# Kernel optimization log

Measured on AMD Instinct MI355X. Metric: run time of the kernel, lower is better.

Reference implementation:

```python
import jax, jax.numpy as jnp
import numpy as np

NHEADS = 8
START_ID = 1
MAX_LEN = 24

def _ln(x, g, b, eps=1e-5):
    m = x.mean(-1, keepdims=True)
    v = ((x - m) ** 2).mean(-1, keepdims=True)
    return (x - m) * jax.lax.rsqrt(v + eps) * g + b

def _mha(q_in, kv_in, w, b, ow, ob, mask):
    # q_in: [Lq,B,E], kv_in: [Lk,B,E]; w: [E,3E] packed q/k/v (transposed torch in_proj)
    E = q_in.shape[-1]; H = NHEADS; D = E // H
    Lq, B = q_in.shape[0], q_in.shape[1]; Lk = kv_in.shape[0]
    q = (q_in @ w[:, :E] + b[:E]).reshape(Lq, B, H, D)
    k = (kv_in @ w[:, E:2 * E] + b[E:2 * E]).reshape(Lk, B, H, D)
    v = (kv_in @ w[:, 2 * E:] + b[2 * E:]).reshape(Lk, B, H, D)
    s = jnp.einsum('qbhd,kbhd->bhqk', q, k) * (1.0 / float(np.sqrt(D)))
    if mask is not None:
        s = s + mask
    a = jax.nn.softmax(s, axis=-1)
    o = jnp.einsum('bhqk,kbhd->qbhd', a, v).reshape(Lq, B, E)
    return o @ ow + ob

def _sinusoidal_pe(S, E):
    pos = np.arange(S)[:, None]
    div = np.exp(np.arange(0, E, 2) * (-np.log(10000.0) / E))
    pe = np.zeros((S, E), dtype=np.float32)
    pe[:, 0::2] = np.sin(pos * div)
    pe[:, 1::2] = np.cos(pos * div)
    return jnp.asarray(pe)[:, None, :]  # [S,1,E]

def _model(input_tensor, emb, enc_attn_w, enc_attn_b, enc_attn_ow, enc_attn_ob,
           enc_ln1_g, enc_ln1_b, enc_ln2_g, enc_ln2_b,
           enc_ffn_w1, enc_ffn_b1, enc_ffn_w2, enc_ffn_b2,
           enc_norm_g, enc_norm_b,
           dec_sa_w, dec_sa_b, dec_sa_ow, dec_sa_ob,
           dec_ca_w, dec_ca_b, dec_ca_ow, dec_ca_ob,
           dec_ln1_g, dec_ln1_b, dec_ln2_g, dec_ln2_b, dec_ln3_g, dec_ln3_b,
           dec_ffn_w1, dec_ffn_b1, dec_ffn_w2, dec_ffn_b2,
           dec_norm_g, dec_norm_b, voc_w, voc_b):
    E = emb.shape[1]
    B, S = input_tensor.shape
    # encoder: seq-first [S,B,E], sinusoidal PE added (decoder side gets NO PE, as in source)
    x = jnp.take(emb, input_tensor.T, axis=0) + _sinusoidal_pe(S, E)
    for l in range(enc_attn_w.shape[0]):  # post-LN encoder layers
        a = _mha(x, x, enc_attn_w[l], enc_attn_b[l], enc_attn_ow[l], enc_attn_ob[l], None)
        x = _ln(x + a, enc_ln1_g[l], enc_ln1_b[l])
        f = jax.nn.relu(x @ enc_ffn_w1[l] + enc_ffn_b1[l]) @ enc_ffn_w2[l] + enc_ffn_b2[l]
        x = _ln(x + f, enc_ln2_g[l], enc_ln2_b[l])
    memory = _ln(x, enc_norm_g, enc_norm_b)

    Lbuf = MAX_LEN + 1
    causal = jnp.where(jnp.triu(jnp.ones((Lbuf, Lbuf), jnp.float32), k=1) == 1, -jnp.inf, 0.0)

    def dec_forward(tokens):
        # full (wasteful, KV-cache-free) decoder pass over the whole token buffer,
        # matching the source's recompute-everything greedy loop; causal masking
        # makes position i identical to the source's length-(i+1) prefix pass.
        y = jnp.take(emb, tokens, axis=0)  # [Lbuf,B,E]; shared embedding, no PE (as in source)
        for l in range(dec_sa_w.shape[0]):
            a = _mha(y, y, dec_sa_w[l], dec_sa_b[l], dec_sa_ow[l], dec_sa_ob[l], causal)
            y = _ln(y + a, dec_ln1_g[l], dec_ln1_b[l])
            c = _mha(y, memory, dec_ca_w[l], dec_ca_b[l], dec_ca_ow[l], dec_ca_ob[l], None)
            y = _ln(y + c, dec_ln2_g[l], dec_ln2_b[l])
            f = jax.nn.relu(y @ dec_ffn_w1[l] + dec_ffn_b1[l]) @ dec_ffn_w2[l] + dec_ffn_b2[l]
            y = _ln(y + f, dec_ln3_g[l], dec_ln3_b[l])
        return _ln(y, dec_norm_g, dec_norm_b)

    def step(tokens, i):
        out_i = jnp.take(dec_forward(tokens), i, axis=0)  # [B,E] == out[-1] of prefix pass
        prob = out_i @ voc_w + voc_b                      # [B,V_tgt]
        nxt = jnp.argmax(prob, axis=-1).astype(tokens.dtype)
        return tokens.at[i + 1].set(nxt), (nxt, prob)

    tokens0 = jnp.full((Lbuf, B), START_ID, dtype=input_tensor.dtype)
    _, (pred_tokens, dists) = jax.lax.scan(step, tokens0, jnp.arange(MAX_LEN))
    return pred_tokens, dists  # [MAX_LEN,B] int, [MAX_LEN,B,V_tgt]


def setup_inputs() -> dict:
    V, VT, E, F, LE, LD, B, S = 32000, 32000, 512, 2048, 3, 3, 8, 24
    keys = iter(jax.random.split(jax.random.key(0), 48))
    def W(*shape):
        return jax.random.normal(next(keys), shape, jnp.float32) * 0.02
    return dict(
        input_tensor=jax.random.randint(next(keys), (B, S), 0, V),
        emb=W(V, E),
        enc_attn_w=W(LE, E, 3 * E), enc_attn_b=jnp.zeros((LE, 3 * E)),
        enc_attn_ow=W(LE, E, E), enc_attn_ob=jnp.zeros((LE, E)),
        enc_ln1_g=jnp.ones((LE, E)), enc_ln1_b=jnp.zeros((LE, E)),
        enc_ln2_g=jnp.ones((LE, E)), enc_ln2_b=jnp.zeros((LE, E)),
        enc_ffn_w1=W(LE, E, F), enc_ffn_b1=jnp.zeros((LE, F)),
        enc_ffn_w2=W(LE, F, E), enc_ffn_b2=jnp.zeros((LE, E)),
        enc_norm_g=jnp.ones((E,)), enc_norm_b=jnp.zeros((E,)),
        dec_sa_w=W(LD, E, 3 * E), dec_sa_b=jnp.zeros((LD, 3 * E)),
        dec_sa_ow=W(LD, E, E), dec_sa_ob=jnp.zeros((LD, E)),
        dec_ca_w=W(LD, E, 3 * E), dec_ca_b=jnp.zeros((LD, 3 * E)),
        dec_ca_ow=W(LD, E, E), dec_ca_ob=jnp.zeros((LD, E)),
        dec_ln1_g=jnp.ones((LD, E)), dec_ln1_b=jnp.zeros((LD, E)),
        dec_ln2_g=jnp.ones((LD, E)), dec_ln2_b=jnp.zeros((LD, E)),
        dec_ln3_g=jnp.ones((LD, E)), dec_ln3_b=jnp.zeros((LD, E)),
        dec_ffn_w1=W(LD, E, F), dec_ffn_b1=jnp.zeros((LD, F)),
        dec_ffn_w2=W(LD, F, E), dec_ffn_b2=jnp.zeros((LD, E)),
        dec_norm_g=jnp.ones((E,)), dec_norm_b=jnp.zeros((E,)),
        voc_w=W(E, VT), voc_b=jnp.zeros((VT,)),
    )


def reference(input_tensor, emb, enc_attn_w, enc_attn_b, enc_attn_ow, enc_attn_ob,
              enc_ln1_g, enc_ln1_b, enc_ln2_g, enc_ln2_b,
              enc_ffn_w1, enc_ffn_b1, enc_ffn_w2, enc_ffn_b2,
              enc_norm_g, enc_norm_b,
              dec_sa_w, dec_sa_b, dec_sa_ow, dec_sa_ob,
              dec_ca_w, dec_ca_b, dec_ca_ow, dec_ca_ob,
              dec_ln1_g, dec_ln1_b, dec_ln2_g, dec_ln2_b, dec_ln3_g, dec_ln3_b,
              dec_ffn_w1, dec_ffn_b1, dec_ffn_w2, dec_ffn_b2,
              dec_norm_g, dec_norm_b, voc_w, voc_b):
    return _model(input_tensor, emb, enc_attn_w, enc_attn_b, enc_attn_ow, enc_attn_ob,
                  enc_ln1_g, enc_ln1_b, enc_ln2_g, enc_ln2_b,
                  enc_ffn_w1, enc_ffn_b1, enc_ffn_w2, enc_ffn_b2,
                  enc_norm_g, enc_norm_b,
                  dec_sa_w, dec_sa_b, dec_sa_ow, dec_sa_ob,
                  dec_ca_w, dec_ca_b, dec_ca_ow, dec_ca_ob,
                  dec_ln1_g, dec_ln1_b, dec_ln2_g, dec_ln2_b, dec_ln3_g, dec_ln3_b,
                  dec_ffn_w1, dec_ffn_b1, dec_ffn_w2, dec_ffn_b2,
                  dec_norm_g, dec_norm_b, voc_w, voc_b)
```

## Files before the change

kernel.cpp:

```cpp
#include <hip/hip_runtime.h>
#include <stdint.h>

#define E    512
#define H    8
#define DH   64
#define BB   8
#define SS   24
#define FF   2048
#define NL   3
#define VTOK 32000
#define LBUF 25
#define ML   24
#define START_ID 1

__global__ void enc_embed_kernel(const int* __restrict__ inp, const float* __restrict__ emb,
                                 float* __restrict__ x) {
  int r = blockIdx.x;
  int s = r / BB, b = r % BB;
  int tok = inp[b * SS + s];
  const float* er = emb + (size_t)tok * E;
  for (int e = threadIdx.x; e < E; e += blockDim.x) {
    int j = e >> 1;
    double dv = exp(-((double)(2 * j)) * (log(10000.0) / (double)E));
    double ang = (double)s * dv;
    double pe = (e & 1) ? cos(ang) : sin(ang);
    x[(size_t)r * E + e] = er[e] + (float)pe;
  }
}

__global__ __launch_bounds__(256) void ln_kernel(const float* __restrict__ x,
                          const float* __restrict__ g,
                          const float* __restrict__ bta, float* __restrict__ y) {
  int r = blockIdx.x;
  int t = threadIdx.x;
  const float* xr = x + (size_t)r * E;
  float a0 = xr[t], a1 = xr[t + 256];
  __shared__ float red[256];
  red[t] = a0 + a1;
  __syncthreads();
  for (int s = 128; s > 0; s >>= 1) { if (t < s) red[t] += red[t + s]; __syncthreads(); }
  float m = red[0] * (1.0f / (float)E);
  __syncthreads();
  float d0 = a0 - m, d1 = a1 - m;
  red[t] = d0 * d0 + d1 * d1;
  __syncthreads();
  for (int s = 128; s > 0; s >>= 1) { if (t < s) red[t] += red[t + s]; __syncthreads(); }
  float v = red[0] * (1.0f / (float)E);
  float rstd = 1.0f / sqrtf(v + 1e-5f);
  y[(size_t)r * E + t]       = d0 * rstd * g[t]       + bta[t];
  y[(size_t)r * E + t + 256] = d1 * rstd * g[t + 256] + bta[t + 256];
}

__global__ __launch_bounds__(256) void fgemm_kernel(
    const float* __restrict__ A, int K,
    const float* __restrict__ W, int ldw, int N,
    const float* __restrict__ bias,
    const float* __restrict__ resid,
    float* __restrict__ C, int relu,
    unsigned long long* __restrict__ amax) {
  __shared__ float Al[8 * 512];
  __shared__ float red[16 * 512];
  int t = threadIdx.x;
  int c0 = blockIdx.x * 64;
  int s = blockIdx.y;
  int row0 = blockIdx.z * 8;
  int kbase = s * 512;
  for (int i = t; i < 1024; i += 256) {
    int r = i >> 7, cc = i & 127;
    ((float4*)Al)[i] = *(const float4*)(A + (size_t)(row0 + r) * K + kbase + (cc << 2));
  }
  __syncthreads();
  int tc = t & 15, tk = t >> 4;
  int col = c0 + (tc << 2);
  float acc[8][4];
#pragma unroll
  for (int m = 0; m < 8; ++m) { acc[m][0] = acc[m][1] = acc[m][2] = acc[m][3] = 0.f; }
  const float4* wp = (const float4*)(W + (size_t)kbase * ldw + col);
  const size_t ld4 = (size_t)(ldw >> 2);
#pragma unroll 8
  for (int i = 0; i < 32; ++i) {
    int k = tk + (i << 4);
    float4 wv = wp[(size_t)k * ld4];
#pragma unroll
    for (int m = 0; m < 8; ++m) {
      float a = Al[m * 512 + k];
      acc[m][0] += a * wv.x; acc[m][1] += a * wv.y;
      acc[m][2] += a * wv.z; acc[m][3] += a * wv.w;
    }
  }
#pragma unroll
  for (int m = 0; m < 8; ++m) {
    float4* rr = (float4*)&red[tk * 512 + m * 64 + (tc << 2)];
    *rr = make_float4(acc[m][0], acc[m][1], acc[m][2], acc[m][3]);
  }
  __syncthreads();
  float out2[2];
#pragma unroll
  for (int j = 0; j < 2; ++j) {
    int o = t + j * 256;
    float v = 0.f;
#pragma unroll
    for (int sl = 0; sl < 16; ++sl) v += red[sl * 512 + o];
    out2[j] = v;
  }
  int S = gridDim.y;
  if (S > 1) {
    int M = gridDim.z * 8;
#pragma unroll
    for (int j = 0; j < 2; ++j) {
      int o = t + j * 256; int m = o >> 6, cc = o & 63;
      C[((size_t)s * M + row0 + m) * N + c0 + cc] = out2[j];
    }
  } else {
#pragma unroll
    for (int j = 0; j < 2; ++j) {
      int o = t + j * 256; int m = o >> 6, cc = o & 63;
      int col2 = c0 + cc;
      float v = out2[j] + bias[col2];
      if (resid) v += resid[(size_t)(row0 + m) * N + col2];
      if (relu) v = fmaxf(v, 0.0f);
      C[(size_t)(row0 + m) * N + col2] = v;
      out2[j] = v;
    }
    if (amax) {
      __syncthreads();
      unsigned long long* keys = (unsigned long long*)red;
// ... 70 lines not shown
  int t = threadIdx.x;
  for (int idx = t; idx < SS * DH; idx += 256) {
    int srow = idx / DH, d = idx - srow * DH;
    size_t base = ((size_t)(srow * BB + b)) * (3 * E) + h * DH + d;
    qs[idx] = qkv[base];
    ks[idx] = qkv[base + E];
    vs[idx] = qkv[base + 2 * E];
  }
  __syncthreads();
  for (int p = t; p < SS * SS; p += 256) {
    int qi = p / SS, kj = p - qi * SS;
    float a = 0.f;
    for (int d = 0; d < DH; ++d) a += qs[qi * DH + d] * ks[kj * DH + d];
    sc[qi][kj] = a * 0.125f;
  }
  __syncthreads();
  if (t < SS) {
    float mx = -1e30f;
    for (int j = 0; j < SS; ++j) mx = fmaxf(mx, sc[t][j]);
    float sm = 0.f;
    for (int j = 0; j < SS; ++j) { float ev = expf(sc[t][j] - mx); sc[t][j] = ev; sm += ev; }
    float inv = 1.0f / sm;
    for (int j = 0; j < SS; ++j) sc[t][j] *= inv;
  }
  __syncthreads();
  for (int p = t; p < SS * DH; p += 256) {
    int qi = p / DH, d = p - qi * DH;
    float a = 0.f;
    for (int j = 0; j < SS; ++j) a += sc[qi][j] * vs[j * DH + d];
    o[((size_t)(qi * BB + b)) * E + h * DH + d] = a;
  }
}

__global__ __launch_bounds__(64) void dec_sa_attn_kernel(const float* __restrict__ qkv,
                                   float* __restrict__ Kc, float* __restrict__ Vc,
                                   float* __restrict__ o, int pos) {
  int b = blockIdx.x >> 3, h = blockIdx.x & 7;
  int t = threadIdx.x;
  const float* qp = qkv + (size_t)b * (3 * E) + h * DH;
  const float* kn = qp + E;
  const float* vn = qp + 2 * E;
  float* kc = Kc + ((size_t)pos * BB + b) * E + h * DH;
  float* vc = Vc + ((size_t)pos * BB + b) * E + h * DH;
  __shared__ float qs[DH];
  __shared__ float sc[32];
  kc[t] = kn[t]; vc[t] = vn[t]; qs[t] = qp[t];
  __syncthreads();
  int L = pos + 1;
  if (t < L) {
    const float* kr = (t == pos) ? kn : (Kc + ((size_t)t * BB + b) * E + h * DH);
    float a = 0.f;
#pragma unroll 8
    for (int d = 0; d < DH; ++d) a += qs[d] * kr[d];
    sc[t] = a * 0.125f;
  }
  __syncthreads();
  if (t == 0) {
    float mx = -1e30f;
    for (int j = 0; j < L; ++j) mx = fmaxf(mx, sc[j]);
    float sm = 0.f;
    for (int j = 0; j < L; ++j) { float ev = expf(sc[j] - mx); sc[j] = ev; sm += ev; }
    float inv = 1.0f / sm;
    for (int j = 0; j < L; ++j) sc[j] *= inv;
  }
  __syncthreads();
  float a = 0.f;
  for (int j = 0; j < L; ++j) {
    const float* vr = (j == pos) ? vn : (Vc + ((size_t)j * BB + b) * E + h * DH);
    a += sc[j] * vr[t];
  }
  o[(size_t)b * E + h * DH + t] = a;
}

__global__ __launch_bounds__(64) void dec_ca_attn_kernel(const float* __restrict__ q,
                                   const float* __restrict__ Km, const float* __restrict__ Vm,
                                   float* __restrict__ o) {
  int b = blockIdx.x >> 3, h = blockIdx.x & 7;
  int t = threadIdx.x;
  __shared__ float qs[DH];
  __shared__ float sc[SS];
  qs[t] = q[(size_t)b * E + h * DH + t];
  __syncthreads();
  if (t < SS) {
    const float* kr = Km + ((size_t)t * BB + b) * E + h * DH;
    float a = 0.f;
#pragma unroll 8
    for (int d = 0; d < DH; ++d) a += qs[d] * kr[d];
    sc[t] = a * 0.125f;
  }
  __syncthreads();
  if (t == 0) {
    float mx = -1e30f;
    for (int j = 0; j < SS; ++j) mx = fmaxf(mx, sc[j]);
    float sm = 0.f;
    for (int j = 0; j < SS; ++j) { float ev = expf(sc[j] - mx); sc[j] = ev; sm += ev; }
    float inv = 1.0f / sm;
    for (int j = 0; j < SS; ++j) sc[j] *= inv;
  }
  __syncthreads();
  float a = 0.f;
  for (int j = 0; j < SS; ++j) a += sc[j] * Vm[((size_t)j * BB + b) * E + h * DH + t];
  o[(size_t)b * E + h * DH + t] = a;
}

__global__ void dec_embed_kernel(const int* __restrict__ tokens, const float* __restrict__ emb,
                                 float* __restrict__ y, int i) {
  int b = blockIdx.x;
  int tok = tokens[i * BB + b];
  const float* er = emb + (size_t)tok * E;
  for (int e = threadIdx.x; e < E; e += blockDim.x) y[(size_t)b * E + e] = er[e];
}

__global__ void dec_init_kernel(int* __restrict__ tokens, unsigned long long* __restrict__ amax) {
  int t = threadIdx.x;
  if (t < BB) { tokens[t] = START_ID; amax[t] = 0ull; }
}

__global__ void next_token_kernel(unsigned long long* __restrict__ amax, int* __restrict__ tokens,
                                  float* __restrict__ outtok, int i) {
  int t = threadIdx.x;
  if (t < BB) {
    unsigned long long p = amax[t];
    int idx = (int)(0xFFFFFFFFu - (unsigned int)(p & 0xFFFFFFFFull));
    tokens[(i + 1) * BB + t] = idx;
    outtok[i * BB + t] = (float)idx;
    amax[t] = 0ull;
  }
}

extern "C" void kernel_launch(void* const* d_in, const int* in_sizes, int n_in,
                              void* d_out, int out_size, void* d_ws, size_t ws_size,
                              hipStream_t stream) {
  (void)in_sizes; (void)n_in; (void)out_size; (void)ws_size;
  const int*   inp   = (const int*)d_in[0];
  const float* emb   = (const float*)d_in[1];
  const float* e_aw  = (const float*)d_in[2];
  const float* e_ab  = (const float*)d_in[3];
  const float* e_aow = (const float*)d_in[4];
  const float* e_aob = (const float*)d_in[5];
  const float* e_l1g = (const float*)d_in[6];
  const float* e_l1b = (const float*)d_in[7];
  const float* e_l2g = (const float*)d_in[8];
  const float* e_l2b = (const float*)d_in[9];
// ... 3 lines not shown
  const float* e_f2b = (const float*)d_in[13];
  const float* e_ng  = (const float*)d_in[14];
  const float* e_nb  = (const float*)d_in[15];
  const float* d_saw = (const float*)d_in[16];
  const float* d_sab = (const float*)d_in[17];
  const float* d_saow= (const float*)d_in[18];
  const float* d_saob= (const float*)d_in[19];
  const float* d_caw = (const float*)d_in[20];
  const float* d_cab = (const float*)d_in[21];
  const float* d_caow= (const float*)d_in[22];
  const float* d_caob= (const float*)d_in[23];
  const float* d_l1g = (const float*)d_in[24];
  const float* d_l1b = (const float*)d_in[25];
  const float* d_l2g = (const float*)d_in[26];
  const float* d_l2b = (const float*)d_in[27];
  const float* d_l3g = (const float*)d_in[28];
  const float* d_l3b = (const float*)d_in[29];
  const float* d_f1w = (const float*)d_in[30];
  const float* d_f1b = (const float*)d_in[31];
  const float* d_f2w = (const float*)d_in[32];
  const float* d_f2b = (const float*)d_in[33];
  const float* d_ng  = (const float*)d_in[34];
  const float* d_nb  = (const float*)d_in[35];
  const float* voc_w = (const float*)d_in[36];
  const float* voc_b = (const float*)d_in[37];
  float* out = (float*)d_out;

  float* p = (float*)d_ws;
  auto alloc = [&](size_t n) { float* r = p; p += n; return r; };
  float* enc_x   = alloc(192 * 512);
  float* enc_tmp = alloc(192 * 2048);
  float* enc_ao  = alloc(192 * 512);
  float* enc_raw = alloc(192 * 512);
  float* memry   = alloc(192 * 512);
  float* mem_k   = alloc(3 * 192 * 512);
  float* mem_v   = alloc(3 * 192 * 512);
  float* partE   = alloc(4 * 192 * 512);
  float* dqkv    = alloc(8 * 1536);
  float* y_in    = alloc(8 * 512);
  float* o_sa    = alloc(8 * 512);
  float* y1      = alloc(8 * 512);
  float* y1raw   = alloc(8 * 512);
  float* qca     = alloc(8 * 512);
  float* oca     = alloc(8 * 512);
  float* y2      = alloc(8 * 512);
  float* y2raw   = alloc(8 * 512);
  float* yf      = alloc(8 * 512);
  float* dmid    = alloc(8 * 2048);
  float* partD   = alloc(4 * 8 * 512);
  float* cacheK  = alloc(3 * LBUF * 8 * 512);
  float* cacheV  = alloc(3 * LBUF * 8 * 512);
  int* tokens    = (int*)alloc(LBUF * 8);
  unsigned long long* amax = (unsigned long long*)alloc(16);

  enc_embed_kernel<<<dim3(192), dim3(256), 0, stream>>>(inp, emb, enc_x);
  for (int l = 0; l < NL; ++l) {
    const float* w  = e_aw  + (size_t)l * E * 3 * E;
    const float* bq = e_ab  + (size_t)l * 3 * E;
    fgemm_kernel<<<dim3(24, 1, 24), dim3(256), 0, stream>>>(
        enc_x, E, w, 3 * E, 3 * E, bq, nullptr, enc_tmp, 0, nullptr);
    enc_attn_kernel<<<dim3(64), dim3(256), 0, stream>>>(enc_tmp, enc_ao);
    fgemm_kernel<<<dim3(8, 1, 24), dim3(256), 0, stream>>>(
        enc_ao, E, e_aow + (size_t)l * E * E, E, E, e_aob + (size_t)l * E,
        enc_x, enc_raw, 0, nullptr);
    ln_kernel<<<dim3(192), dim3(256), 0, stream>>>(enc_raw, e_l1g + l * E, e_l1b + l * E, enc_x);
    fgemm_kernel<<<dim3(32, 1, 24), dim3(256), 0, stream>>>(
        enc_x, E, e_f1w + (size_t)l * E * FF, FF, FF, e_f1b + (size_t)l * FF,
        nullptr, enc_tmp, 1, nullptr);
    fgemm_kernel<<<dim3(8, 4, 24), dim3(256), 0, stream>>>(
        enc_tmp, FF, e_f2w + (size_t)l * FF * E, E, E, nullptr,
        nullptr, partE, 0, nullptr);
    reduce_br_kernel<<<dim3(192), dim3(256), 0, stream>>>(
        partE, 4, 192, e_f2b + (size_t)l * E, enc_x, enc_raw);
    ln_kernel<<<dim3(192), dim3(256), 0, stream>>>(enc_raw, e_l2g + l * E, e_l2b + l * E, enc_x);
  }
  ln_kernel<<<dim3(192), dim3(256), 0, stream>>>(enc_x, e_ng, e_nb, memry);

  for (int l = 0; l < NL; ++l) {
    const float* w  = d_caw + (size_t)l * E * 3 * E;
    const float* bq = d_cab + (size_t)l * 3 * E;
    fgemm_kernel<<<dim3(8, 1, 24), dim3(256), 0, stream>>>(
        memry, E, w + E, 3 * E, E, bq + E, nullptr,
        mem_k + (size_t)l * 192 * 512, 0, nullptr);
    fgemm_kernel<<<dim3(8, 1, 24), dim3(256), 0, stream>>>(
        memry, E, w + 2 * E, 3 * E, E, bq + 2 * E, nullptr,
        mem_v + (size_t)l * 192 * 512, 0, nullptr);
  }

  dec_init_kernel<<<dim3(1), dim3(64), 0, stream>>>(tokens, amax);
  for (int i = 0; i < ML; ++i) {
    dec_embed_kernel<<<dim3(8), dim3(256), 0, stream>>>(tokens, emb, y_in, i);
    for (int l = 0; l < NL; ++l) {
      const float* saw = d_saw + (size_t)l * E * 3 * E;
      const float* sab = d_sab + (size_t)l * 3 * E;
      const float* caw = d_caw + (size_t)l * E * 3 * E;
      const float* cab = d_cab + (size_t)l * 3 * E;
      float* Kc = cacheK + (size_t)l * LBUF * 8 * 512;
      float* Vc = cacheV + (size_t)l * LBUF * 8 * 512;

      fgemm_kernel<<<dim3(24, 1, 1), dim3(256), 0, stream>>>(
          y_in, E, saw, 3 * E, 3 * E, sab, nullptr, dqkv, 0, nullptr);
      dec_sa_attn_kernel<<<dim3(64), dim3(64), 0, stream>>>(dqkv, Kc, Vc, o_sa, i);
      fgemm_kernel<<<dim3(8, 1, 1), dim3(256), 0, stream>>>(
          o_sa, E, d_saow + (size_t)l * E * E, E, E, d_saob + (size_t)l * E,
          y_in, y1raw, 0, nullptr);
      ln_kernel<<<dim3(8), dim3(256), 0, stream>>>(y1raw, d_l1g + l * E, d_l1b + l * E, y1);

      fgemm_kernel<<<dim3(8, 1, 1), dim3(256), 0, stream>>>(
          y1, E, caw, 3 * E, E, cab, nullptr, qca, 0, nullptr);
      dec_ca_attn_kernel<<<dim3(64), dim3(64), 0, stream>>>(
          qca, mem_k + (size_t)l * 192 * 512, mem_v + (size_t)l * 192 * 512, oca);
      fgemm_kernel<<<dim3(8, 1, 1), dim3(256), 0, stream>>>(
          oca, E, d_caow + (size_t)l * E * E, E, E, d_caob + (size_t)l * E,
          y1, y2raw, 0, nullptr);
      ln_kernel<<<dim3(8), dim3(256), 0, stream>>>(y2raw, d_l2g + l * E, d_l2b + l * E, y2);

      fgemm_kernel<<<dim3(32, 1, 1), dim3(256), 0, stream>>>(
          y2, E, d_f1w + (size_t)l * E * FF, FF, FF, d_f1b + (size_t)l * FF,
          nullptr, dmid, 1, nullptr);
      fgemm_kernel<<<dim3(8, 4, 1), dim3(256), 0, stream>>>(
          dmid, FF, d_f2w + (size_t)l * FF * E, E, E, nullptr,
          nullptr, partD, 0, nullptr);
      reduce_ln_kernel<<<dim3(8), dim3(256), 0, stream>>>(
          partD, 4, d_f2b + (size_t)l * E, y2, d_l3g + l * E, d_l3b + l * E, y_in);
    }
    ln_kernel<<<dim3(8), dim3(256), 0, stream>>>(y_in, d_ng, d_nb, yf);

    float* dist_i = out + 192 + (size_t)i * (8 * VTOK);
    fgemm_kernel<<<dim3(500, 1, 1), dim3(256), 0, stream>>>(
        yf, E, voc_w, VTOK, VTOK, voc_b, nullptr, dist_i, 0, amax);
    next_token_kernel<<<dim3(1), dim3(64), 0, stream>>>(amax, tokens, out, i);
  }
}
```

Before: 6.030 ms.

## Fuse decoder LayerNorms, embedding, attention and output projections into GEMM prologues

Decoder-step kernels are merged. The token embedding gather, the FFN partial-sum reduction with residual, and the LayerNorms now run as prologues of the following GEMM. Self- and cross-attention are each fused with their output projection into single 8-block kernels. The goal is fewer tiny launches per decode step in this launch-bound loop, at the cost of every GEMM block recomputing the LayerNorm and attention redundantly, and of the fused attention running on only 8 blocks.

```diff
diff --git a/kernel.cpp b/kernel.cpp
--- a/kernel.cpp
+++ b/kernel.cpp
@@ -57,19 +57,71 @@
     const float* __restrict__ bias,
     const float* __restrict__ resid,
     float* __restrict__ C, int relu,
-    unsigned long long* __restrict__ amax) {
+    unsigned long long* __restrict__ amax,
+    const float* __restrict__ lng, const float* __restrict__ lnb,
+    float* __restrict__ astore,
+    const int* __restrict__ gtok, const float* __restrict__ gemb,
+    const float* __restrict__ rpart, const float* __restrict__ rbias,
+    const float* __restrict__ rresid) {
   __shared__ float Al[8 * 512];
   __shared__ float red[16 * 512];
+  __shared__ float rm[8], rrs[8];
   int t = threadIdx.x;
   int c0 = blockIdx.x * 64;
   int s = blockIdx.y;
   int row0 = blockIdx.z * 8;
   int kbase = s * 512;
-  for (int i = t; i < 1024; i += 256) {
-    int r = i >> 7, cc = i & 127;
-    ((float4*)Al)[i] = *(const float4*)(A + (size_t)(row0 + r) * K + kbase + (cc << 2));
-  }
-  __syncthreads();
+  if (gtok) {
+    for (int i = t; i < 1024; i += 256) {
+      int r = i >> 7, cc = i & 127;
+      int tok = gtok[r];
+      ((float4*)Al)[i] = *(const float4*)(gemb + (size_t)tok * E + (cc << 2));
+    }
+  } else if (rpart) {
+    for (int i = t; i < 1024; i += 256) {
+      int r = i >> 7, cc = i & 127;
+      int c = cc << 2;
+      float4 v = *(const float4*)(rbias + c);
+      float4 rv = *(const float4*)(rresid + (size_t)r * E + c);
+      v.x += rv.x; v.y += rv.y; v.z += rv.z; v.w += rv.w;
+      for (int sl = 0; sl < 4; ++sl) {
+        float4 pv = *(const float4*)(rpart + ((size_t)sl * 8 + r) * E + c);
+        v.x += pv.x; v.y += pv.y; v.z += pv.z; v.w += pv.w;
+      }
+      ((float4*)Al)[i] = v;
+    }
+  } else {
+    for (int i = t; i < 1024; i += 256) {
+      int r = i >> 7, cc = i & 127;
+      ((float4*)Al)[i] = *(const float4*)(A + (size_t)(row0 + r) * K + kbase + (cc << 2));
+    }
+  }
+  __syncthreads();
+  if (lng) {
+    int rr = t >> 5, q = t & 31;
+    const float* ar = Al + rr * 512;
+    float sm = 0.f, s2 = 0.f;
+    for (int j = q; j < 512; j += 32) { float v = ar[j]; sm += v; s2 += v * v; }
+    for (int off = 16; off; off >>= 1) {
+      sm += __shfl_down(sm, off, 32);
+      s2 += __shfl_down(s2, off, 32);
+    }
+    if (q == 0) {
+      float m = sm * (1.0f / 512.0f);
+      float var = s2 * (1.0f / 512.0f) - m * m;
+      rm[rr] = m;
+      rrs[rr] = 1.0f / sqrtf(var + 1e-5f);
+    }
+    __syncthreads();
+    for (int idx = t; idx < 4096; idx += 256) {
+      int r2 = idx >> 9, c2 = idx & 511;
+      Al[idx] = (Al[idx] - rm[r2]) * rrs[r2] * lng[c2] + lnb[c2];
+    }
+    __syncthreads();
+  }
+  if (astore && blockIdx.x == 0 && blockIdx.y == 0) {
+    for (int idx = t; idx < 4096; idx += 256) astore[idx] = Al[idx];
+  }
   int tc = t & 15, tk = t >> 4;
   int col = c0 + (tc << 2);
   float acc[8][4];
@@ -90,8 +142,8 @@
   }
 #pragma unroll
   for (int m = 0; m < 8; ++m) {
-    float4* rr = (float4*)&red[tk * 512 + m * 64 + (tc << 2)];
-    *rr = make_float4(acc[m][0], acc[m][1], acc[m][2], acc[m][3]);
+    float4* rr2 = (float4*)&red[tk * 512 + m * 64 + (tc << 2)];
+    *rr2 = make_float4(acc[m][0], acc[m][1], acc[m][2], acc[m][3]);
   }
   __syncthreads();
   float out2[2];
@@ -228,83 +280,185 @@
   }
 }
 
-__global__ __launch_bounds__(64) void dec_sa_attn_kernel(const float* __restrict__ qkv,
-                                   float* __restrict__ Kc, float* __restrict__ Vc,
-                                   float* __restrict__ o, int pos) {
-  int b = blockIdx.x >> 3, h = blockIdx.x & 7;
+__global__ __launch_bounds__(256) void dec_sa_ow_kernel(
+    const float* __restrict__ qkv,
+    float* __restrict__ Kc, float* __restrict__ Vc, int pos,
+    const float* __restrict__ W,
+    const float* __restrict__ bias,
+    const float* __restrict__ resid,
+    float* __restrict__ C) {
+  __shared__ float Ao[8 * 512];
+  __shared__ float red[16 * 512];
+  __shared__ float sc[64][25];
   int t = threadIdx.x;
-  const float* qp = qkv + (size_t)b * (3 * E) + h * DH;
-  const float* kn = qp + E;
-  const float* vn = qp + 2 * E;
-  float* kc = Kc + ((size_t)pos * BB + b) * E + h * DH;
-  float* vc = Vc + ((size_t)pos * BB + b) * E + h * DH;
-  __shared__ float qs[DH];
-  __shared__ float sc[32];
-  kc[t] = kn[t]; vc[t] = vn[t]; qs[t] = qp[t];
-  __syncthreads();
   int L = pos + 1;
-  if (t < L) {
-    const float* kr = (t == pos) ? kn : (Kc + ((size_t)t * BB + b) * E + h * DH);
+  if (blockIdx.x == 0) {
+    for (int idx = t; idx < 4096; idx += 256) {
+      int b = idx >> 9, e = idx & 511;
+      const float* row = qkv + (size_t)b * 1536;
+      Kc[((size_t)pos * BB + b) * E + e] = row[512 + e];
+      Vc[((size_t)pos * BB + b) * E + e] = row[1024 + e];
+    }
+  }
+  {
+    int p = t >> 2, q = t & 3;
+    int b = p >> 3, h = p & 7;
+    const float4* q4 = (const float4*)(qkv + (size_t)b * 1536 + h * 64);
+    for (int j = q; j < L; j += 4) {
+      const float* kr = (j == pos) ? (qkv + (size_t)b * 1536 + 512 + h * 64)
+                                   : (Kc + ((size_t)j * BB + b) * E + h * 64);
+      const float4* k4 = (const float4*)kr;
+      float a = 0.f;
+#pragma unroll
+      for (int d = 0; d < 16; ++d) {
+        float4 qv = q4[d], kv = k4[d];
+        a += qv.x * kv.x + qv.y * kv.y + qv.z * kv.z + qv.w * kv.w;
+      }
+      sc[p][j] = a * 0.125f;
+    }
+  }
+  __syncthreads();
+  if ((t & 3) == 0) {
+    int p = t >> 2;
+    float mx = -1e30f;
+    for (int j = 0; j < L; ++j) mx = fmaxf(mx, sc[p][j]);
+    float sm = 0.f;
+    for (int j = 0; j < L; ++j) { float ev = expf(sc[p][j] - mx); sc[p][j] = ev; sm += ev; }
+    float inv = 1.0f / sm;
+    for (int j = 0; j < L; ++j) sc[p][j] *= inv;
+  }
+  __syncthreads();
+  for (int ii = 0; ii < 16; ++ii) {
+    int idx = t + (ii << 8);
+    int b = idx >> 9, e = idx & 511, h = e >> 6;
+    int p = b * 8 + h;
     float a = 0.f;
+    for (int j = 0; j < L; ++j) {
+      float vv = (j == pos) ? qkv[(size_t)b * 1536 + 1024 + e]
+                            : Vc[((size_t)j * BB + b) * E + e];
+      a += sc[p][j] * vv;
+    }
+    Ao[idx] = a;
+  }
+  __syncthreads();
+  int tc = t & 15, tk = t >> 4;
+  int c0 = blockIdx.x * 64;
+  int col = c0 + (tc << 2);
+  float acc[8][4];
+#pragma unroll
+  for (int m = 0; m < 8; ++m) { acc[m][0] = acc[m][1] = acc[m][2] = acc[m][3] = 0.f; }
+  const float4* wp = (const float4*)(W + col);
 #pragma unroll 8
-    for (int d = 0; d < DH; ++d) a += qs[d] * kr[d];
-    sc[t] = a * 0.125f;
-  }
-  __syncthreads();
-  if (t == 0) {
+  for (int i = 0; i < 32; ++i) {
+    int k = tk + (i << 4);
+    float4 wv = wp[(size_t)k * 128];
+#pragma unroll
+    for (int m = 0; m < 8; ++m) {
+      float a = Ao[m * 512 + k];
+      acc[m][0] += a * wv.x; acc[m][1] += a * wv.y;
+      acc[m][2] += a * wv.z; acc[m][3] += a * wv.w;
+    }
+  }
+#pragma unroll
+  for (int m = 0; m < 8; ++m) {
+    float4* rr = (float4*)&red[tk * 512 + m * 64 + (tc << 2)];
+    *rr = make_float4(acc[m][0], acc[m][1], acc[m][2], acc[m][3]);
+  }
+  __syncthreads();
+#pragma unroll
+  for (int j = 0; j < 2; ++j) {
+    int o = t + j * 256;
+    float v = 0.f;
+#pragma unroll
+    for (int sl = 0; sl < 16; ++sl) v += red[sl * 512 + o];
+    int m = o >> 6, cc = o & 63;
+    int col2 = c0 + cc;
+    v += bias[col2] + resid[(size_t)m * E + col2];
+    C[(size_t)m * E + col2] = v;
+  }
+}
+
+__global__ __launch_bounds__(256) void dec_ca_ow_kernel(
+    const float* __restrict__ qvec,
+    const float* __restrict__ Km, const float* __restrict__ Vm,
+    const float* __restrict__ W,
+    const float* __restrict__ bias,
+    const float* __restrict__ resid,
+    float* __restrict__ C) {
+  __shared__ float Ao[8 * 512];
+  __shared__ float red[16 * 512];
+  __shared__ float sc[64][25];
+  int t = threadIdx.x;
+  {
+    int p = t >> 2, q = t & 3;
+    int b = p >> 3, h = p & 7;
+    const float4* q4 = (const float4*)(qvec + (size_t)b * E + h * 64);
+    for (int j = q; j < SS; j += 4) {
+      const float4* k4 = (const float4*)(Km + ((size_t)j * BB + b) * E + h * 64);
+      float a = 0.f;
+#pragma unroll
+      for (int d = 0; d < 16; ++d) {
+        float4 qv = q4[d], kv = k4[d];
+        a += qv.x * kv.x + qv.y * kv.y + qv.z * kv.z + qv.w * kv.w;
+      }
+      sc[p][j] = a * 0.125f;
+    }
+  }
+  __syncthreads();
+  if ((t & 3) == 0) {
+    int p = t >> 2;
     float mx = -1e30f;
-    for (int j = 0; j < L; ++j) mx = fmaxf(mx, sc[j]);
+    for (int j = 0; j < SS; ++j) mx = fmaxf(mx, sc[p][j]);
     float sm = 0.f;
-    for (int j = 0; j < L; ++j) { float ev = expf(sc[j] - mx); sc[j] = ev; sm += ev; }
+    for (int j = 0; j < SS; ++j) { float ev = expf(sc[p][j] - mx); sc[p][j] = ev; sm += ev; }
     float inv = 1.0f / sm;
-    for (int j = 0; j < L; ++j) sc[j] *= inv;
-  }
-  __syncthreads();
-  float a = 0.f;
-  for (int j = 0; j < L; ++j) {
-    const float* vr = (j == pos) ? vn : (Vc + ((size_t)j * BB + b) * E + h * DH);
-    a += sc[j] * vr[t];
-  }
-  o[(size_t)b * E + h * DH + t] = a;
-}
-
-__global__ __launch_bounds__(64) void dec_ca_attn_kernel(const float* __restrict__ q,
-                                   const float* __restrict__ Km, const float* __restrict__ Vm,
-                                   float* __restrict__ o) {
-  int b = blockIdx.x >> 3, h = blockIdx.x & 7;
-  int t = threadIdx.x;
-  __shared__ float qs[DH];
-  __shared__ float sc[SS];
-  qs[t] = q[(size_t)b * E + h * DH + t];
-  __syncthreads();
-  if (t < SS) {
-    const float* kr = Km + ((size_t)t * BB + b) * E + h * DH;
+    for (int j = 0; j < SS; ++j) sc[p][j] *= inv;
+  }
+  __syncthreads();
+  for (int ii = 0; ii < 16; ++ii) {
+    int idx = t + (ii << 8);
+    int b = idx >> 9, e = idx & 511, h = e >> 6;
+    int p = b * 8 + h;
     float a = 0.f;
+    for (int j = 0; j < SS; ++j) a += sc[p][j] * Vm[((size_t)j * BB + b) * E + e];
+    Ao[idx] = a;
+  }
+  __syncthreads();
+  int tc = t & 15, tk = t >> 4;
+  int c0 = blockIdx.x * 64;
+  int col = c0 + (tc << 2);
+  float acc[8][4];
+#pragma unroll
+  for (int m = 0; m < 8; ++m) { acc[m][0] = acc[m][1] = acc[m][2] = acc[m][3] = 0.f; }
+  const float4* wp = (const float4*)(W + col);
 #pragma unroll 8
-    for (int d = 0; d < DH; ++d) a += qs[d] * kr[d];
-    sc[t] = a * 0.125f;
-  }
-  __syncthreads();
-  if (t == 0) {
-    float mx = -1e30f;
-    for (int j = 0; j < SS; ++j) mx = fmaxf(mx, sc[j]);
-    float sm = 0.f;
-    for (int j = 0; j < SS; ++j) { float ev = expf(sc[j] - mx); sc[j] = ev; sm += ev; }
-    float inv = 1.0f / sm;
-    for (int j = 0; j < SS; ++j) sc[j] *= inv;
-  }
-  __syncthreads();
-  float a = 0.f;
-  for (int j = 0; j < SS; ++j) a += sc[j] * Vm[((size_t)j * BB + b) * E + h * DH + t];
-  o[(size_t)b * E + h * DH + t] = a;
-}
-
-__global__ void dec_embed_kernel(const int* __restrict__ tokens, const float* __restrict__ emb,
-                                 float* __restrict__ y, int i) {
-  int b = blockIdx.x;
-  int tok = tokens[i * BB + b];
-  const float* er = emb + (size_t)tok * E;
-  for (int e = threadIdx.x; e < E; e += blockDim.x) y[(size_t)b * E + e] = er[e];
+  for (int i = 0; i < 32; ++i) {
+    int k = tk + (i << 4);
+    float4 wv = wp[(size_t)k * 128];
+#pragma unroll
+    for (int m = 0; m < 8; ++m) {
+      float a = Ao[m * 512 + k];
+      acc[m][0] += a * wv.x; acc[m][1] += a * wv.y;
+      acc[m][2] += a * wv.z; acc[m][3] += a * wv.w;
+    }
+  }
+#pragma unroll
+  for (int m = 0; m < 8; ++m) {
+    float4* rr = (float4*)&red[tk * 512 + m * 64 + (tc << 2)];
+    *rr = make_float4(acc[m][0], acc[m][1], acc[m][2], acc[m][3]);
+  }
+  __syncthreads();
+#pragma unroll
+  for (int j = 0; j < 2; ++j) {
+    int o = t + j * 256;
+    float v = 0.f;
+#pragma unroll
+    for (int sl = 0; sl < 16; ++sl) v += red[sl * 512 + o];
+    int m = o >> 6, cc = o & 63;
+    int col2 = c0 + cc;
+    v += bias[col2] + resid[(size_t)m * E + col2];
+    C[(size_t)m * E + col2] = v;
+  }
 }
 
 __global__ void dec_init_kernel(int* __restrict__ tokens, unsigned long long* __restrict__ amax) {
@@ -380,14 +534,11 @@
   float* partE   = alloc(4 * 192 * 512);
   float* dqkv    = alloc(8 * 1536);
   float* y_in    = alloc(8 * 512);
-  float* o_sa    = alloc(8 * 512);
   float* y1      = alloc(8 * 512);
   float* y1raw   = alloc(8 * 512);
   float* qca     = alloc(8 * 512);
-  float* oca     = alloc(8 * 512);
   float* y2      = alloc(8 * 512);
   float* y2raw   = alloc(8 * 512);
-  float* yf      = alloc(8 * 512);
   float* dmid    = alloc(8 * 2048);
   float* partD   = alloc(4 * 8 * 512);
   float* cacheK  = alloc(3 * LBUF * 8 * 512);
@@ -395,23 +546,25 @@
   int* tokens    = (int*)alloc(LBUF * 8);
   unsigned long long* amax = (unsigned long long*)alloc(16);
 
+#define FG_NULLS nullptr, nullptr, nullptr, nullptr, nullptr, nullptr, nullptr, nullptr
+
   enc_embed_kernel<<<dim3(192), dim3(256), 0, stream>>>(inp, emb, enc_x);
   for (int l = 0; l < NL; ++l) {
     const float* w  = e_aw  + (size_t)l * E * 3 * E;
     const float* bq = e_ab  + (size_t)l * 3 * E;
     fgemm_kernel<<<dim3(24, 1, 24), dim3(256), 0, stream>>>(
-        enc_x, E, w, 3 * E, 3 * E, bq, nullptr, enc_tmp, 0, nullptr);
+        enc_x, E, w, 3 * E, 3 * E, bq, nullptr, enc_tmp, 0, nullptr, FG_NULLS);
     enc_attn_kernel<<<dim3(64), dim3(256), 0, stream>>>(enc_tmp, enc_ao);
     fgemm_kernel<<<dim3(8, 1, 24), dim3(256), 0, stream>>>(
         enc_ao, E, e_aow + (size_t)l * E * E, E, E, e_aob + (size_t)l * E,
-        enc_x, enc_raw, 0, nullptr);
+        enc_x, enc_raw, 0, nullptr, FG_NULLS);
     ln_kernel<<<dim3(192), dim3(256), 0, stream>>>(enc_raw, e_l1g + l * E, e_l1b + l * E, enc_x);
     fgemm_kernel<<<dim3(32, 1, 24), dim3(256), 0, stream>>>(
         enc_x, E, e_f1w + (size_t)l * E * FF, FF, FF, e_f1b + (size_t)l * FF,
-        nullptr, enc_tmp, 1, nullptr);
+        nullptr, enc_tmp, 1, nullptr, FG_NULLS);
     fgemm_kernel<<<dim3(8, 4, 24), dim3(256), 0, stream>>>(
         enc_tmp, FF, e_f2w + (size_t)l * FF * E, E, E, nullptr,
-        nullptr, partE, 0, nullptr);
+        nullptr, partE, 0, nullptr, FG_NULLS);
     reduce_br_kernel<<<dim3(192), dim3(256), 0, stream>>>(
         partE, 4, 192, e_f2b + (size_t)l * E, enc_x, enc_raw);
     ln_kernel<<<dim3(192), dim3(256), 0, stream>>>(enc_raw, e_l2g + l * E, e_l2b + l * E, enc_x);
@@ -423,15 +576,14 @@
     const float* bq = d_cab + (size_t)l * 3 * E;
     fgemm_kernel<<<dim3(8, 1, 24), dim3(256), 0, stream>>>(
         memry, E, w + E, 3 * E, E, bq + E, nullptr,
-        mem_k + (size_t)l * 192 * 512, 0, nullptr);
+        mem_k + (size_t)l * 192 * 512, 0, nullptr, FG_NULLS);
     fgemm_kernel<<<dim3(8, 1, 24), dim3(256), 0, stream>>>(
         memry, E, w + 2 * E, 3 * E, E, bq + 2 * E, nullptr,
-        mem_v + (size_t)l * 192 * 512, 0, nullptr);
+        mem_v + (size_t)l * 192 * 512, 0, nullptr, FG_NULLS);
   }
 
   dec_init_kernel<<<dim3(1), dim3(64), 0, stream>>>(tokens, amax);
   for (int i = 0; i < ML; ++i) {
-    dec_embed_kernel<<<dim3(8), dim3(256), 0, stream>>>(tokens, emb, y_in, i);
     for (int l = 0; l < NL; ++l) {
       const float* saw = d_saw + (size_t)l * E * 3 * E;
       const float* sab = d_sab + (size_t)l * 3 * E;
@@ -440,37 +592,47 @@
       float* Kc = cacheK + (size_t)l * LBUF * 8 * 512;
       float* Vc = cacheV + (size_t)l * LBUF * 8 * 512;
 
-      fgemm_kernel<<<dim3(24, 1, 1), dim3(256), 0, stream>>>(
-          y_in, E, saw, 3 * E, 3 * E, sab, nullptr, dqkv, 0, nullptr);
-      dec_sa_attn_kernel<<<dim3(64), dim3(64), 0, stream>>>(dqkv, Kc, Vc, o_sa, i);
+      if (l == 0) {
+        fgemm_kernel<<<dim3(24, 1, 1), dim3(256), 0, stream>>>(
+            nullptr, E, saw, 3 * E, 3 * E, sab, nullptr, dqkv, 0, nullptr,
+            nullptr, nullptr, y_in,
+            tokens + (size_t)i * BB, emb,
+            nullptr, nullptr, nullptr);
+      } else {
+        fgemm_kernel<<<dim3(24, 1, 1), dim3(256), 0, stream>>>(
+            nullptr, E, saw, 3 * E, 3 * E, sab, nullptr, dqkv, 0, nullptr,
+            d_l3g + (size_t)(l - 1) * E, d_l3b + (size_t)(l - 1) * E, y_in,
+            nullptr, nullptr,
+            partD, d_f2b + (size_t)(l - 1) * E, y2);
+      }
+      dec_sa_ow_kernel<<<dim3(8), dim3(256), 0, stream>>>(
+          dqkv, Kc, Vc, i, d_saow + (size_t)l * E * E, d_saob + (size_t)l * E,
+          y_in, y1raw);
       fgemm_kernel<<<dim3(8, 1, 1), dim3(256), 0, stream>>>(
-          o_sa, E, d_saow + (size_t)l * E * E, E, E, d_saob + (size_t)l * E,
-          y_in, y1raw, 0, nullptr);
-      ln_kernel<<<dim3(8), dim3(256), 0, stream>>>(y1raw, d_l1g + l * E, d_l1b + l * E, y1);
-
-      fgemm_kernel<<<dim3(8, 1, 1), dim3(256), 0, stream>>>(
-          y1, E, caw, 3 * E, E, cab, nullptr, qca, 0, nullptr);
-      dec_ca_attn_kernel<<<dim3(64), dim3(64), 0, stream>>>(
-          qca, mem_k + (size_t)l * 192 * 512, mem_v + (size_t)l * 192 * 512, oca);
-      fgemm_kernel<<<dim3(8, 1, 1), dim3(256), 0, stream>>>(
-          oca, E, d_caow + (size_t)l * E * E, E, E, d_caob + (size_t)l * E,
-          y1, y2raw, 0, nullptr);
-      ln_kernel<<<dim3(8), dim3(256), 0, stream>>>(y2raw, d_l2g + l * E, d_l2b + l * E, y2);
-
+          y1raw, E, caw, 3 * E, E, cab, nullptr, qca, 0, nullptr,
+          d_l1g + (size_t)l * E, d_l1b + (size_t)l * E, y1,
+          nullptr, nullptr, nullptr, nullptr, nullptr);
+      dec_ca_ow_kernel<<<dim3(8), dim3(256), 0, stream>>>(
+          qca, mem_k + (size_t)l * 192 * 512, mem_v + (size_t)l * 192 * 512,
+          d_caow + (size_t)l * E * E, d_caob + (size_t)l * E, y1, y2raw);
       fgemm_kernel<<<dim3(32, 1, 1), dim3(256), 0, stream>>>(
-          y2, E, d_f1w + (size_t)l * E * FF, FF, FF, d_f1b + (size_t)l * FF,
-          nullptr, dmid, 1, nullptr);
+          y2raw, E, d_f1w + (size_t)l * E * FF, FF, FF, d_f1b + (size_t)l * FF,
+          nullptr, dmid, 1, nullptr,
+          d_l2g + (size_t)l * E, d_l2b + (size_t)l * E, y2,
+          nullptr, nullptr, nullptr, nullptr, nullptr);
       fgemm_kernel<<<dim3(8, 4, 1), dim3(256), 0, stream>>>(
           dmid, FF, d_f2w + (size_t)l * FF * E, E, E, nullptr,
-          nullptr, partD, 0, nullptr);
-      reduce_ln_kernel<<<dim3(8), dim3(256), 0, stream>>>(
-          partD, 4, d_f2b + (size_t)l * E, y2, d_l3g + l * E, d_l3b + l * E, y_in);
-    }
-    ln_kernel<<<dim3(8), dim3(256), 0, stream>>>(y_in, d_ng, d_nb, yf);
+          nullptr, partD, 0, nullptr, FG_NULLS);
+    }
+    reduce_ln_kernel<<<dim3(8), dim3(256), 0, stream>>>(
+        partD, 4, d_f2b + (size_t)(NL - 1) * E, y2,
+        d_l3g + (size_t)(NL - 1) * E, d_l3b + (size_t)(NL - 1) * E, y_in);
 
     float* dist_i = out + 192 + (size_t)i * (8 * VTOK);
     fgemm_kernel<<<dim3(500, 1, 1), dim3(256), 0, stream>>>(
-        yf, E, voc_w, VTOK, VTOK, voc_b, nullptr, dist_i, 0, amax);
+        y_in, E, voc_w, VTOK, VTOK, voc_b, nullptr, dist_i, 0, amax,
+        d_ng, d_nb, nullptr, nullptr, nullptr, nullptr, nullptr, nullptr);
     next_token_kernel<<<dim3(1), dim3(64), 0, stream>>>(amax, tokens, out, i);
   }
-}
+#undef FG_NULLS
+}
```

After: 8.865 ms (median of 2 runs). +47.0%, slower.

## Fuse LayerNorm, embedding gather and split-K reduce into GEMM A-tile prologue

Applied to the files above, without the earlier changes.

Removes the standalone LayerNorm kernels, the decoder embedding kernel and most reduce_ln launches. Each GEMM now normalizes its 8-row A tile in shared memory, gathers embeddings, or sums the split-K partials with bias and residual while loading. One block writes the normalized tile back so it can serve as the next residual. This cuts many small launches in the latency-bound decode loop, at the cost of every block recomputing the LayerNorm on its tile, an extra branchy prologue, and single-pass variance (E[x²]−m²) replacing the two-pass form.

```diff
diff --git a/kernel.cpp b/kernel.cpp
--- a/kernel.cpp
+++ b/kernel.cpp
@@ -28,27 +28,30 @@
   }
 }
 
-__global__ __launch_bounds__(256) void ln_kernel(const float* __restrict__ x,
-                          const float* __restrict__ g,
-                          const float* __restrict__ bta, float* __restrict__ y) {
-  int r = blockIdx.x;
-  int t = threadIdx.x;
-  const float* xr = x + (size_t)r * E;
-  float a0 = xr[t], a1 = xr[t + 256];
-  __shared__ float red[256];
-  red[t] = a0 + a1;
-  __syncthreads();
-  for (int s = 128; s > 0; s >>= 1) { if (t < s) red[t] += red[t + s]; __syncthreads(); }
-  float m = red[0] * (1.0f / (float)E);
-  __syncthreads();
-  float d0 = a0 - m, d1 = a1 - m;
-  red[t] = d0 * d0 + d1 * d1;
-  __syncthreads();
-  for (int s = 128; s > 0; s >>= 1) { if (t < s) red[t] += red[t + s]; __syncthreads(); }
-  float v = red[0] * (1.0f / (float)E);
-  float rstd = 1.0f / sqrtf(v + 1e-5f);
-  y[(size_t)r * E + t]       = d0 * rstd * g[t]       + bta[t];
-  y[(size_t)r * E + t + 256] = d1 * rstd * g[t + 256] + bta[t + 256];
+__device__ __forceinline__ void ln_tile(float* Al, const float* __restrict__ g,
+                                        const float* __restrict__ b,
+                                        float* rm, float* rrs) {
+  int t = threadIdx.x;
+  int rr = t >> 5, q = t & 31;
+  const float* ar = Al + rr * 512;
+  float sm = 0.f, s2 = 0.f;
+  for (int j = q; j < 512; j += 32) { float v = ar[j]; sm += v; s2 += v * v; }
+  for (int off = 16; off; off >>= 1) {
+    sm += __shfl_down(sm, off, 32);
+    s2 += __shfl_down(s2, off, 32);
+  }
+  if (q == 0) {
+    float m = sm * (1.0f / 512.0f);
+    float var = s2 * (1.0f / 512.0f) - m * m;
+    rm[rr] = m;
+    rrs[rr] = 1.0f / sqrtf(var + 1e-5f);
+  }
+  __syncthreads();
+  for (int idx = t; idx < 4096; idx += 256) {
+    int r2 = idx >> 9, c2 = idx & 511;
+    Al[idx] = (Al[idx] - rm[r2]) * rrs[r2] * g[c2] + b[c2];
+  }
+  __syncthreads();
 }
 
 __global__ __launch_bounds__(256) void fgemm_kernel(
@@ -57,19 +60,55 @@
     const float* __restrict__ bias,
     const float* __restrict__ resid,
     float* __restrict__ C, int relu,
-    unsigned long long* __restrict__ amax) {
+    unsigned long long* __restrict__ amax,
+    const float* __restrict__ lng, const float* __restrict__ lnb,
+    const float* __restrict__ lng2, const float* __restrict__ lnb2,
+    float* __restrict__ astore,
+    const int* __restrict__ gtok, const float* __restrict__ gemb,
+    const float* __restrict__ rpart, const float* __restrict__ rbias,
+    const float* __restrict__ rresid) {
   __shared__ float Al[8 * 512];
   __shared__ float red[16 * 512];
+  __shared__ float rm[8], rrs[8];
   int t = threadIdx.x;
   int c0 = blockIdx.x * 64;
   int s = blockIdx.y;
   int row0 = blockIdx.z * 8;
   int kbase = s * 512;
-  for (int i = t; i < 1024; i += 256) {
-    int r = i >> 7, cc = i & 127;
-    ((float4*)Al)[i] = *(const float4*)(A + (size_t)(row0 + r) * K + kbase + (cc << 2));
-  }
-  __syncthreads();
+  if (gtok) {
+    for (int i = t; i < 1024; i += 256) {
+      int r = i >> 7, cc = i & 127;
+      int tok = gtok[r];
+      ((float4*)Al)[i] = *(const float4*)(gemb + (size_t)tok * E + (cc << 2));
+    }
+  } else if (rpart) {
+    for (int i = t; i < 1024; i += 256) {
+      int r = i >> 7, cc = i & 127;
+      int c = cc << 2;
+      float4 v = *(const float4*)(rbias + c);
+      float4 rv = *(const float4*)(rresid + (size_t)r * E + c);
+      v.x += rv.x; v.y += rv.y; v.z += rv.z; v.w += rv.w;
+      for (int sl = 0; sl < 4; ++sl) {
+        float4 pv = *(const float4*)(rpart + ((size_t)sl * 8 + r) * E + c);
+        v.x += pv.x; v.y += pv.y; v.z += pv.z; v.w += pv.w;
+      }
+      ((float4*)Al)[i] = v;
+    }
+  } else {
+    for (int i = t; i < 1024; i += 256) {
+      int r = i >> 7, cc = i & 127;
+      ((float4*)Al)[i] = *(const float4*)(A + (size_t)(row0 + r) * K + kbase + (cc << 2));
+    }
+  }
+  __syncthreads();
+  if (lng) {
+    ln_tile(Al, lng, lnb, rm, rrs);
+    if (lng2) ln_tile(Al, lng2, lnb2, rm, rrs);
+  }
+  if (astore && blockIdx.x == 0 && blockIdx.y == 0) {
+    float* ap = astore + (size_t)row0 * 512;
+    for (int idx = t; idx < 4096; idx += 256) ap[idx] = Al[idx];
+  }
   int tc = t & 15, tk = t >> 4;
   int col = c0 + (tc << 2);
   float acc[8][4];
@@ -90,8 +129,8 @@
   }
 #pragma unroll
   for (int m = 0; m < 8; ++m) {
-    float4* rr = (float4*)&red[tk * 512 + m * 64 + (tc << 2)];
-    *rr = make_float4(acc[m][0], acc[m][1], acc[m][2], acc[m][3]);
+    float4* rr2 = (float4*)&red[tk * 512 + m * 64 + (tc << 2)];
+    *rr2 = make_float4(acc[m][0], acc[m][1], acc[m][2], acc[m][3]);
   }
   __syncthreads();
   float out2[2];
@@ -297,14 +336,6 @@
   float a = 0.f;
   for (int j = 0; j < SS; ++j) a += sc[j] * Vm[((size_t)j * BB + b) * E + h * DH + t];
   o[(size_t)b * E + h * DH + t] = a;
-}
-
-__global__ void dec_embed_kernel(const int* __restrict__ tokens, const float* __restrict__ emb,
-                                 float* __restrict__ y, int i) {
-  int b = blockIdx.x;
-  int tok = tokens[i * BB + b];
-  const float* er = emb + (size_t)tok * E;
-  for (int e = threadIdx.x; e < E; e += blockDim.x) y[(size_t)b * E + e] = er[e];
 }
 
 __global__ void dec_init_kernel(int* __restrict__ tokens, unsigned long long* __restrict__ amax) {
@@ -374,7 +405,6 @@
   float* enc_tmp = alloc(192 * 2048);
   float* enc_ao  = alloc(192 * 512);
   float* enc_raw = alloc(192 * 512);
-  float* memry   = alloc(192 * 512);
   float* mem_k   = alloc(3 * 192 * 512);
   float* mem_v   = alloc(3 * 192 * 512);
   float* partE   = alloc(4 * 192 * 512);
@@ -387,7 +417,6 @@
   float* oca     = alloc(8 * 512);
   float* y2      = alloc(8 * 512);
   float* y2raw   = alloc(8 * 512);
-  float* yf      = alloc(8 * 512);
   float* dmid    = alloc(8 * 2048);
   float* partD   = alloc(4 * 8 * 512);
   float* cacheK  = alloc(3 * LBUF * 8 * 512);
@@ -395,43 +424,58 @@
   int* tokens    = (int*)alloc(LBUF * 8);
   unsigned long long* amax = (unsigned long long*)alloc(16);
 
+#define FGZ nullptr, nullptr, nullptr, nullptr, nullptr, nullptr, nullptr, nullptr, nullptr, nullptr, nullptr
+
   enc_embed_kernel<<<dim3(192), dim3(256), 0, stream>>>(inp, emb, enc_x);
   for (int l = 0; l < NL; ++l) {
     const float* w  = e_aw  + (size_t)l * E * 3 * E;
     const float* bq = e_ab  + (size_t)l * 3 * E;
-    fgemm_kernel<<<dim3(24, 1, 24), dim3(256), 0, stream>>>(
-        enc_x, E, w, 3 * E, 3 * E, bq, nullptr, enc_tmp, 0, nullptr);
+    if (l == 0) {
+      fgemm_kernel<<<dim3(24, 1, 24), dim3(256), 0, stream>>>(
+          enc_x, E, w, 3 * E, 3 * E, bq, nullptr, enc_tmp, 0, FGZ);
+    } else {
+      fgemm_kernel<<<dim3(24, 1, 24), dim3(256), 0, stream>>>(
+          enc_raw, E, w, 3 * E, 3 * E, bq, nullptr, enc_tmp, 0,
+          nullptr, e_l2g + (size_t)(l - 1) * E, e_l2b + (size_t)(l - 1) * E,
+          nullptr, nullptr, enc_x,
+          nullptr, nullptr, nullptr, nullptr, nullptr);
+    }
     enc_attn_kernel<<<dim3(64), dim3(256), 0, stream>>>(enc_tmp, enc_ao);
     fgemm_kernel<<<dim3(8, 1, 24), dim3(256), 0, stream>>>(
         enc_ao, E, e_aow + (size_t)l * E * E, E, E, e_aob + (size_t)l * E,
-        enc_x, enc_raw, 0, nullptr);
-    ln_kernel<<<dim3(192), dim3(256), 0, stream>>>(enc_raw, e_l1g + l * E, e_l1b + l * E, enc_x);
+        enc_x, enc_raw, 0, FGZ);
     fgemm_kernel<<<dim3(32, 1, 24), dim3(256), 0, stream>>>(
-        enc_x, E, e_f1w + (size_t)l * E * FF, FF, FF, e_f1b + (size_t)l * FF,
-        nullptr, enc_tmp, 1, nullptr);
+        enc_raw, E, e_f1w + (size_t)l * E * FF, FF, FF, e_f1b + (size_t)l * FF,
+        nullptr, enc_tmp, 1,
+        nullptr, e_l1g + (size_t)l * E, e_l1b + (size_t)l * E,
+        nullptr, nullptr, enc_x,
+        nullptr, nullptr, nullptr, nullptr, nullptr);
     fgemm_kernel<<<dim3(8, 4, 24), dim3(256), 0, stream>>>(
         enc_tmp, FF, e_f2w + (size_t)l * FF * E, E, E, nullptr,
-        nullptr, partE, 0, nullptr);
+        nullptr, partE, 0, FGZ);
     reduce_br_kernel<<<dim3(192), dim3(256), 0, stream>>>(
         partE, 4, 192, e_f2b + (size_t)l * E, enc_x, enc_raw);
-    ln_kernel<<<dim3(192), dim3(256), 0, stream>>>(enc_raw, e_l2g + l * E, e_l2b + l * E, enc_x);
-  }
-  ln_kernel<<<dim3(192), dim3(256), 0, stream>>>(enc_x, e_ng, e_nb, memry);
+  }
 
   for (int l = 0; l < NL; ++l) {
     const float* w  = d_caw + (size_t)l * E * 3 * E;
     const float* bq = d_cab + (size_t)l * 3 * E;
     fgemm_kernel<<<dim3(8, 1, 24), dim3(256), 0, stream>>>(
-        memry, E, w + E, 3 * E, E, bq + E, nullptr,
-        mem_k + (size_t)l * 192 * 512, 0, nullptr);
+        enc_raw, E, w + E, 3 * E, E, bq + E, nullptr,
+        mem_k + (size_t)l * 192 * 512, 0,
+        nullptr, e_l2g + (size_t)2 * E, e_l2b + (size_t)2 * E,
+        e_ng, e_nb, nullptr,
+        nullptr, nullptr, nullptr, nullptr, nullptr);
     fgemm_kernel<<<dim3(8, 1, 24), dim3(256), 0, stream>>>(
-        memry, E, w + 2 * E, 3 * E, E, bq + 2 * E, nullptr,
-        mem_v + (size_t)l * 192 * 512, 0, nullptr);
+        enc_raw, E, w + 2 * E, 3 * E, E, bq + 2 * E, nullptr,
+        mem_v + (size_t)l * 192 * 512, 0,
+        nullptr, e_l2g + (size_t)2 * E, e_l2b + (size_t)2 * E,
+        e_ng, e_nb, nullptr,
+        nullptr, nullptr, nullptr, nullptr, nullptr);
   }
 
   dec_init_kernel<<<dim3(1), dim3(64), 0, stream>>>(tokens, amax);
   for (int i = 0; i < ML; ++i) {
-    dec_embed_kernel<<<dim3(8), dim3(256), 0, stream>>>(tokens, emb, y_in, i);
     for (int l = 0; l < NL; ++l) {
       const float* saw = d_saw + (size_t)l * E * 3 * E;
       const float* sab = d_sab + (size_t)l * 3 * E;
@@ -440,37 +484,54 @@
       float* Kc = cacheK + (size_t)l * LBUF * 8 * 512;
       float* Vc = cacheV + (size_t)l * LBUF * 8 * 512;
 
-      fgemm_kernel<<<dim3(24, 1, 1), dim3(256), 0, stream>>>(
-          y_in, E, saw, 3 * E, 3 * E, sab, nullptr, dqkv, 0, nullptr);
+      if (l == 0) {
+        fgemm_kernel<<<dim3(24, 1, 1), dim3(256), 0, stream>>>(
+            nullptr, E, saw, 3 * E, 3 * E, sab, nullptr, dqkv, 0,
+            nullptr, nullptr, nullptr, nullptr, nullptr, y_in,
+            tokens + (size_t)i * BB, emb,
+            nullptr, nullptr, nullptr);
+      } else {
+        fgemm_kernel<<<dim3(24, 1, 1), dim3(256), 0, stream>>>(
+            nullptr, E, saw, 3 * E, 3 * E, sab, nullptr, dqkv, 0,
+            nullptr, d_l3g + (size_t)(l - 1) * E, d_l3b + (size_t)(l - 1) * E,
+            nullptr, nullptr, y_in,
+            nullptr, nullptr,
+            partD, d_f2b + (size_t)(l - 1) * E, y2);
+      }
       dec_sa_attn_kernel<<<dim3(64), dim3(64), 0, stream>>>(dqkv, Kc, Vc, o_sa, i);
       fgemm_kernel<<<dim3(8, 1, 1), dim3(256), 0, stream>>>(
           o_sa, E, d_saow + (size_t)l * E * E, E, E, d_saob + (size_t)l * E,
-          y_in, y1raw, 0, nullptr);
-      ln_kernel<<<dim3(8), dim3(256), 0, stream>>>(y1raw, d_l1g + l * E, d_l1b + l * E, y1);
-
+          y_in, y1raw, 0, FGZ);
       fgemm_kernel<<<dim3(8, 1, 1), dim3(256), 0, stream>>>(
-          y1, E, caw, 3 * E, E, cab, nullptr, qca, 0, nullptr);
+          y1raw, E, caw, 3 * E, E, cab, nullptr, qca, 0,
+          nullptr, d_l1g + (size_t)l * E, d_l1b + (size_t)l * E,
+          nullptr, nullptr, y1,
+          nullptr, nullptr, nullptr, nullptr, nullptr);
       dec_ca_attn_kernel<<<dim3(64), dim3(64), 0, stream>>>(
           qca, mem_k + (size_t)l * 192 * 512, mem_v + (size_t)l * 192 * 512, oca);
       fgemm_kernel<<<dim3(8, 1, 1), dim3(256), 0, stream>>>(
           oca, E, d_caow + (size_t)l * E * E, E, E, d_caob + (size_t)l * E,
-          y1, y2raw, 0, nullptr);
-      ln_kernel<<<dim3(8), dim3(256), 0, stream>>>(y2raw, d_l2g + l * E, d_l2b + l * E, y2);
-
+          y1, y2raw, 0, FGZ);
       fgemm_kernel<<<dim3(32, 1, 1), dim3(256), 0, stream>>>(
-          y2, E, d_f1w + (size_t)l * E * FF, FF, FF, d_f1b + (size_t)l * FF,
-          nullptr, dmid, 1, nullptr);
+          y2raw, E, d_f1w + (size_t)l * E * FF, FF, FF, d_f1b + (size_t)l * FF,
+          nullptr, dmid, 1,
+          nullptr, d_l2g + (size_t)l * E, d_l2b + (size_t)l * E,
+          nullptr, nullptr, y2,
+          nullptr, nullptr, nullptr, nullptr, nullptr);
       fgemm_kernel<<<dim3(8, 4, 1), dim3(256), 0, stream>>>(
           dmid, FF, d_f2w + (size_t)l * FF * E, E, E, nullptr,
-          nullptr, partD, 0, nullptr);
-      reduce_ln_kernel<<<dim3(8), dim3(256), 0, stream>>>(
-          partD, 4, d_f2b + (size_t)l * E, y2, d_l3g + l * E, d_l3b + l * E, y_in);
-    }
-    ln_kernel<<<dim3(8), dim3(256), 0, stream>>>(y_in, d_ng, d_nb, yf);
+          nullptr, partD, 0, FGZ);
+    }
+    reduce_ln_kernel<<<dim3(8), dim3(256), 0, stream>>>(
+        partD, 4, d_f2b + (size_t)(NL - 1) * E, y2,
+        d_l3g + (size_t)(NL - 1) * E, d_l3b + (size_t)(NL - 1) * E, y_in);
 
     float* dist_i = out + 192 + (size_t)i * (8 * VTOK);
     fgemm_kernel<<<dim3(500, 1, 1), dim3(256), 0, stream>>>(
-        yf, E, voc_w, VTOK, VTOK, voc_b, nullptr, dist_i, 0, amax);
+        y_in, E, voc_w, VTOK, VTOK, voc_b, nullptr, dist_i, 0,
+        amax, d_ng, d_nb, nullptr, nullptr, nullptr,
+        nullptr, nullptr, nullptr, nullptr, nullptr);
     next_token_kernel<<<dim3(1), dim3(64), 0, stream>>>(amax, tokens, out, i);
   }
-}
+#undef FGZ
+}
```

Result: slower. 6.219 ms (+3.1%).
